# Optimization experiments

Measured on AMD Instinct MI355X. Metric: run time of the kernel, lower is better.

Reference implementation:

```python
import jax, jax.numpy as jnp
import numpy as np

BS, N = 32, 512
NHALF = N // 2            # mapped atoms per sample (half reactant, half product)
IN_X, IN_E, IN_C, IN_BD = 16, 5, 3, 3
OUT_X, OUT_E, OUT_C, OUT_BD = 16, 5, 3, 3


def setup_inputs() -> dict:
    key = jax.random.key(0)
    k = jax.random.split(key, 6)
    X = jax.random.normal(k[0], (BS, N, IN_X), dtype=jnp.float32)
    E = jax.random.normal(k[1], (BS, N, N, IN_E), dtype=jnp.float32)
    atom_charges = jax.random.normal(k[2], (BS, N, IN_C), dtype=jnp.float32)
    bond_dirs = jax.random.normal(k[3], (BS, N, N, IN_BD), dtype=jnp.float32)
    # atom map numbers: reactant half and product half each carry a permutation of 1..NHALF
    rk = jax.random.split(k[4], BS)
    pk = jax.random.split(k[5], BS)
    rct_amn = jax.vmap(lambda kk: jax.random.permutation(kk, NHALF))(rk).astype(jnp.int32) + 1
    prod_amn = jax.vmap(lambda kk: jax.random.permutation(kk, NHALF))(pk).astype(jnp.int32) + 1
    atom_map_numbers = jnp.concatenate([rct_amn, prod_amn], axis=1)  # [BS,N]
    mol_assignment = jnp.concatenate([
        jnp.ones((BS, NHALF), jnp.int32),       # reactant atoms
        jnp.full((BS, NHALF), 2, jnp.int32),    # product atoms (max assignment)
    ], axis=1)
    return {"X": X, "E": E, "atom_charges": atom_charges, "bond_dirs": bond_dirs,
            "atom_map_numbers": atom_map_numbers, "mol_assignment": mol_assignment}


def _alignment_maps(atom_map_numbers, mol_assignment):
    """Vectorized equivalent of the per-sample python loops: for each reactant
    position j with atom-map number m>0 (present among product atoms), find the
    product position carrying the same m ('correct' alignment_type)."""
    bs, n = atom_map_numbers.shape
    bidx = jnp.arange(bs)[:, None]
    prod_assign = mol_assignment.max(axis=-1, keepdims=True)
    amn_prod = jnp.where(mol_assignment == prod_assign, atom_map_numbers, 0)  # [bs,n]
    amn_rct = jnp.where(mol_assignment < prod_assign, atom_map_numbers, 0)
    # rowwise_atom_mapping_mask: keep only rct numbers present in prod row
    present = jnp.zeros((bs, n + 1), bool).at[bidx, amn_prod].set(True)
    present = present.at[:, 0].set(False)
    amn_rct = jnp.where(jnp.take_along_axis(present, amn_rct, axis=1), amn_rct, 0)
    # inverse table: prodpos_table[i,m] = product position j with amn_prod[i,j]==m
    pos = jnp.broadcast_to(jnp.arange(n, dtype=jnp.int32), (bs, n))
    prodpos_table = jnp.zeros((bs, n + 1), jnp.int32).at[bidx, amn_prod].set(pos)
    prodpos = jnp.take_along_axis(prodpos_table, amn_rct, axis=1)  # [bs,n]
    mask = amn_rct > 0  # reactant positions that received aligned product features
    return prodpos, mask


def _gather_pairs(T, p):
    # T: [bs,n,n,d], p: [bs,n] -> T[i, p[j1], p[j2], :]
    return jax.vmap(lambda Ti, pi: Ti[pi][:, pi])(T, p)


def reference(X, E, atom_charges, bond_dirs, atom_map_numbers, mol_assignment):
    prodpos, mask = _alignment_maps(atom_map_numbers, mol_assignment)
    m1 = mask[..., None].astype(X.dtype)
    pair = (mask[:, :, None] & mask[:, None, :])  # [bs,n,n]
    pairf = pair[..., None].astype(X.dtype)

    # node-feature alignment (gather product features, scatter to reactant slots)
    Xg = jnp.take_along_axis(X[..., :OUT_X], prodpos[..., None], axis=1) * m1
    Cg = jnp.take_along_axis(atom_charges[..., :OUT_C], prodpos[..., None], axis=1) * m1

    # edge-feature alignment
    E1 = _gather_pairs(E[..., :OUT_E], prodpos) * pairf          # aligned product edges
    onehot0 = jax.nn.one_hot(0, E.shape[-1], dtype=X.dtype)
    E2 = (1.0 - pairf) * onehot0                                  # skip conn on non-mapped pairs
    BD1 = _gather_pairs(bond_dirs[..., :OUT_BD], prodpos) * pairf

    X_cat = jnp.concatenate([X, Xg], axis=-1)
    C_cat = jnp.concatenate([atom_charges, Cg], axis=-1)
    return (X_cat, C_cat, E1, E2, BD1)
```

## Files before the change

kernel.cpp:

```cpp
#include <hip/hip_runtime.h>
#include <hip/hip_bf16.h>

#define BSZ 32
#define NN  512

static const long O_XC = 0;
static const long O_CC = 524288L;
static const long O_E1 = 622592L;
static const long O_E2 = 42565632L;
static const long O_BD = 84508672L;

__global__ __launch_bounds__(NN) void align_kernel(
    const int* __restrict__ amn, const int* __restrict__ ma,
    int* __restrict__ p2m)
{
    const int i = blockIdx.x;
    const int t = threadIdx.x;

    __shared__ int red[NN];
    __shared__ int table[NN + 1];

    const int a = ma[i * NN + t];
    red[t] = a;
    __syncthreads();
    for (int s = NN / 2; s > 0; s >>= 1) {
        if (t < s) red[t] = max(red[t], red[t + s]);
        __syncthreads();
    }
    const int prod_assign = red[0];

    table[t] = -1;
    if (t == 0) table[NN] = -1;
    __syncthreads();

    const int m = amn[i * NN + t];
    if (a == prod_assign && m > 0 && m <= NN) table[m] = t;
    __syncthreads();

    int p = -1;
    if (a < prod_assign && m > 0 && m <= NN) p = table[m];
    p2m[i * NN + t] = p;
}

__global__ __launch_bounds__(256) void node_kernel(
    const float* __restrict__ X,
    const float* __restrict__ AC,
    const int* __restrict__ p2m,
    float* __restrict__ out)
{
    const int idx = blockIdx.x * 256 + threadIdx.x;
    if (idx >= BSZ * NN) return;
    const int i = idx >> 9;
    const int p = p2m[idx];

    const float4* xr4 = (const float4*)(X + (size_t)idx * 16);
    float4* ox4 = (float4*)(out + O_XC + (size_t)idx * 32);
#pragma unroll
    for (int c = 0; c < 4; ++c) ox4[c] = xr4[c];
    if (p >= 0) {
        const float4* xp4 = (const float4*)(X + ((size_t)i * NN + p) * 16);
#pragma unroll
        for (int c = 0; c < 4; ++c) ox4[4 + c] = xp4[c];
    } else {
        const float4 z = make_float4(0.f, 0.f, 0.f, 0.f);
#pragma unroll
        for (int c = 0; c < 4; ++c) ox4[4 + c] = z;
    }

    const float* cr = AC + (size_t)idx * 3;
    float* oc = out + O_CC + (size_t)idx * 6;
#pragma unroll
    for (int c = 0; c < 3; ++c) oc[c] = cr[c];
    if (p >= 0) {
        const float* cp = AC + ((size_t)i * NN + p) * 3;
#pragma unroll
        for (int c = 0; c < 3; ++c) oc[3 + c] = cp[c];
    } else {
#pragma unroll
        for (int c = 0; c < 3; ++c) oc[3 + c] = 0.0f;
    }
}

__global__ __launch_bounds__(NN) void edge_kernel(
    const float* __restrict__ E,
    const float* __restrict__ BD,
    const int* __restrict__ p2m,
    float* __restrict__ out)
{
    const int b  = blockIdx.x;
    const int i  = b >> 9;
    const int j1 = b & (NN - 1);
    const int t  = threadIdx.x;

    __shared__ int sp[NN];
    sp[t] = p2m[i * NN + t];
    __syncthreads();

    const int p1  = sp[j1];
    const int p1c = p1 < 0 ? 0 : p1;
    const float* __restrict__ Erow = E  + ((size_t)i * NN + p1c) * NN * 5;
    const float* __restrict__ Brow = BD + ((size_t)i * NN + p1c) * NN * 3;

    float4* oE1 = (float4*)(out + O_E1 + (size_t)b * (NN * 5));
    float4* oE2 = (float4*)(out + O_E2 + (size_t)b * (NN * 5));
    float4* oBD = (float4*)(out + O_BD + (size_t)b * (NN * 3));

    for (int f = t; f < 640; f += NN) {
        float4 v;
        float* vv = (float*)&v;
#pragma unroll
        for (int k = 0; k < 4; ++k) {
            const int g  = 4 * f + k;
            const int j2 = g / 5;
            const int c  = g - j2 * 5;
            const int p2 = sp[j2];
            float x = 0.0f;
            if (p1 >= 0 && p2 >= 0) x = Erow[p2 * 5 + c];
            vv[k] = x;
        }
        oE1[f] = v;
    }

    for (int f = t; f < 640; f += NN) {
        float4 v;
        float* vv = (float*)&v;
#pragma unroll
        for (int k = 0; k < 4; ++k) {
            const int g  = 4 * f + k;
            const int j2 = g / 5;
            const int c  = g - j2 * 5;
            const int p2 = sp[j2];
            vv[k] = (p1 >= 0 && p2 >= 0) ? 0.0f : (c == 0 ? 1.0f : 0.0f);
        }
        oE2[f] = v;
    }

    for (int f = t; f < 384; f += NN) {
        float4 v;
        float* vv = (float*)&v;
#pragma unroll
        for (int k = 0; k < 4; ++k) {
            const int g  = 4 * f + k;
            const int j2 = g / 3;
            const int c  = g - j2 * 3;
            const int p2 = sp[j2];
            float x = 0.0f;
            if (p1 >= 0 && p2 >= 0) x = Brow[p2 * 3 + c];
            vv[k] = x;
        }
        oBD[f] = v;
    }
}

extern "C" void kernel_launch(void* const* d_in, const int* in_sizes, int n_in,
                              void* d_out, int out_size, void* d_ws, size_t ws_size,
                              hipStream_t stream) {
    const float* X  = (const float*)d_in[0];
    const float* E  = (const float*)d_in[1];
    const float* AC = (const float*)d_in[2];
    const float* BD = (const float*)d_in[3];
    const int* amn = (const int*)d_in[4];
    const int* ma  = (const int*)d_in[5];
    float* out = (float*)d_out;

    int* p2m = (int*)d_ws;

    align_kernel<<<BSZ, NN, 0, stream>>>(amn, ma, p2m);
    node_kernel<<<(BSZ * NN + 255) / 256, 256, 0, stream>>>(X, AC, p2m, out);
    edge_kernel<<<BSZ * NN, NN, 0, stream>>>(E, BD, p2m, out);
}
```

Before: 574.4 us.

## Stage gathered edge rows in LDS, early-exit unmapped rows, use nontemporal stores

```diff
diff --git a/kernel.cpp b/kernel.cpp
--- a/kernel.cpp
+++ b/kernel.cpp
@@ -9,6 +9,8 @@
 static const long O_E1 = 622592L;
 static const long O_E2 = 42565632L;
 static const long O_BD = 84508672L;
+
+typedef float f32x4 __attribute__((ext_vector_type(4)));
 
 __global__ __launch_bounds__(NN) void align_kernel(
     const int* __restrict__ amn, const int* __restrict__ ma,
@@ -92,63 +94,78 @@
     const int j1 = b & (NN - 1);
     const int t  = threadIdx.x;
 
-    __shared__ int sp[NN];
+    f32x4* oE1 = (f32x4*)(out + O_E1 + (size_t)b * (NN * 5));
+    f32x4* oE2 = (f32x4*)(out + O_E2 + (size_t)b * (NN * 5));
+    f32x4* oBD = (f32x4*)(out + O_BD + (size_t)b * (NN * 3));
+
+    __shared__ int   sp[NN];
+    __shared__ float sE[NN * 5];
+    __shared__ float sB[NN * 3];
+
+    const int p1 = p2m[i * NN + j1];
+
+    if (p1 < 0) {
+        const f32x4 z = {0.f, 0.f, 0.f, 0.f};
+        for (int f = t; f < 640; f += NN) {
+            f32x4 v2;
+#pragma unroll
+            for (int k = 0; k < 4; ++k) {
+                const int g  = 4 * f + k;
+                const int j2 = g / 5;
+                const int c  = g - j2 * 5;
+                v2[k] = (c == 0) ? 1.0f : 0.0f;
+            }
+            __builtin_nontemporal_store(z,  oE1 + f);
+            __builtin_nontemporal_store(v2, oE2 + f);
+        }
+        for (int f = t; f < 384; f += NN)
+            __builtin_nontemporal_store(z, oBD + f);
+        return;
+    }
+
     sp[t] = p2m[i * NN + t];
+    {
+        const f32x4* Er4 = (const f32x4*)(E  + ((size_t)i * NN + p1) * (NN * 5));
+        const f32x4* Br4 = (const f32x4*)(BD + ((size_t)i * NN + p1) * (NN * 3));
+        f32x4* sE4 = (f32x4*)sE;
+        f32x4* sB4 = (f32x4*)sB;
+        sE4[t] = Er4[t];
+        if (t < 128) sE4[NN + t] = Er4[NN + t];
+        if (t < 384) sB4[t] = Br4[t];
+    }
     __syncthreads();
 
-    const int p1  = sp[j1];
-    const int p1c = p1 < 0 ? 0 : p1;
-    const float* __restrict__ Erow = E  + ((size_t)i * NN + p1c) * NN * 5;
-    const float* __restrict__ Brow = BD + ((size_t)i * NN + p1c) * NN * 3;
-
-    float4* oE1 = (float4*)(out + O_E1 + (size_t)b * (NN * 5));
-    float4* oE2 = (float4*)(out + O_E2 + (size_t)b * (NN * 5));
-    float4* oBD = (float4*)(out + O_BD + (size_t)b * (NN * 3));
-
     for (int f = t; f < 640; f += NN) {
-        float4 v;
-        float* vv = (float*)&v;
+        f32x4 v1, v2;
 #pragma unroll
         for (int k = 0; k < 4; ++k) {
-            const int g  = 4 * f + k;
-            const int j2 = g / 5;
-            const int c  = g - j2 * 5;
-            const int p2 = sp[j2];
-            float x = 0.0f;
-            if (p1 >= 0 && p2 >= 0) x = Erow[p2 * 5 + c];
-            vv[k] = x;
+            const int g   = 4 * f + k;
+            const int j2  = g / 5;
+            const int c   = g - j2 * 5;
+            const int p2  = sp[j2];
+            const int p2c = p2 < 0 ? 0 : p2;
+            const float e = sE[p2c * 5 + c];
+            const bool pair = (p2 >= 0);
+            v1[k] = pair ? e : 0.0f;
+            v2[k] = pair ? 0.0f : (c == 0 ? 1.0f : 0.0f);
         }
-        oE1[f] = v;
-    }
-
-    for (int f = t; f < 640; f += NN) {
-        float4 v;
-        float* vv = (float*)&v;
-#pragma unroll
-        for (int k = 0; k < 4; ++k) {
-            const int g  = 4 * f + k;
-            const int j2 = g / 5;
-            const int c  = g - j2 * 5;
-            const int p2 = sp[j2];
-            vv[k] = (p1 >= 0 && p2 >= 0) ? 0.0f : (c == 0 ? 1.0f : 0.0f);
-        }
-        oE2[f] = v;
+        __builtin_nontemporal_store(v1, oE1 + f);
+        __builtin_nontemporal_store(v2, oE2 + f);
     }
 
     for (int f = t; f < 384; f += NN) {
-        float4 v;
-        float* vv = (float*)&v;
+        f32x4 v;
 #pragma unroll
         for (int k = 0; k < 4; ++k) {
-            const int g  = 4 * f + k;
-            const int j2 = g / 3;
-            const int c  = g - j2 * 3;
-            const int p2 = sp[j2];
-            float x = 0.0f;
-            if (p1 >= 0 && p2 >= 0) x = Brow[p2 * 3 + c];
-            vv[k] = x;
+            const int g   = 4 * f + k;
+            const int j2  = g / 3;
+            const int c   = g - j2 * 3;
+            const int p2  = sp[j2];
+            const int p2c = p2 < 0 ? 0 : p2;
+            const float x = sB[p2c * 3 + c];
+            v[k] = (p2 >= 0) ? x : 0.0f;
         }
-        oBD[f] = v;
+        __builtin_nontemporal_store(v, oBD + f);
     }
 }
 
```

After: 594.2 us. +3.4%, slower.
